# Performance work log

Measured on AMD Instinct MI355X. Metric: run time of the kernel, lower is better.

The kernel has to match this reference:

```python
import jax, jax.numpy as jnp
import numpy as np

B = 4            # scenes
N = 100000       # points per scene
BN = B * N
M = 200000       # occupied target voxels
C_IMG = 64       # img_feat_dim
C_3D = 32        # INIT_DIM (3D feature width at p1 scale)
COORD_MAX = 256  # voxel grid extent per axis


def setup_inputs() -> dict:
    key = jax.random.key(0)
    k1, k2, k3, k4, k5, k6 = jax.random.split(key, 6)
    # batched voxel coords: col0 = batch idx, cols1:4 = xyz voxel coords
    bcol = jax.random.randint(k1, (M, 1), 0, B, dtype=jnp.int32)
    xyz = jax.random.randint(k2, (M, 3), 0, COORD_MAX, dtype=jnp.int32)
    tgt_coords = jnp.concatenate([bcol, xyz], axis=1)  # (M,4)
    # each point maps onto some target voxel (torch code asserts full validity)
    pts_idx = jax.random.randint(k3, (BN,), 0, M, dtype=jnp.int32)
    pfeat = jax.random.normal(k4, (BN, C_IMG), dtype=jnp.float32)
    tgt_feats = jax.random.normal(k5, (M, C_3D), dtype=jnp.float32)
    W_fuse = jax.random.normal(k6, (C_3D + C_IMG, C_3D), dtype=jnp.float32) * 0.05
    b_fuse = jnp.zeros((C_3D,), dtype=jnp.float32)
    return {"pfeat": pfeat, "tgt_feats": tgt_feats, "W_fuse": W_fuse,
            "b_fuse": b_fuse, "tgt_coords": tgt_coords, "pts_idx": pts_idx}


def reference(pfeat, tgt_feats, W_fuse, b_fuse, tgt_coords, pts_idx):
    # point voxel coords (stride-snapped in torch; identity here since points map to voxels)
    pts_coords = tgt_coords[pts_idx]                              # (BN,4)
    # --- key packing (mirrors _pack_keys with shift-to-nonnegative) ---
    xyz_all = jnp.concatenate([pts_coords[:, 1:], tgt_coords[:, 1:]], axis=0)
    shift = jnp.maximum(-xyz_all.min(axis=0), 0)
    pts_xyz = pts_coords[:, 1:] + shift
    tgt_xyz = tgt_coords[:, 1:] + shift
    max_xyz = jnp.maximum(pts_xyz.max(axis=0), tgt_xyz.max(axis=0))
    mx, my, mz = max_xyz[0] + 1, max_xyz[1] + 1, max_xyz[2] + 1

    def pack(b, xyz):
        return ((b * mx + xyz[:, 0]) * my + xyz[:, 1]) * mz + xyz[:, 2]

    pts_key = pack(pts_coords[:, 0], pts_xyz)                     # (BN,)
    tgt_key = pack(tgt_coords[:, 0], tgt_xyz)                     # (M,)
    # --- sort target keys, binary-search point keys (torch.sort + searchsorted) ---
    order = jnp.argsort(tgt_key)
    tgt_key_sorted = tgt_key[order]
    pos = jnp.minimum(jnp.searchsorted(tgt_key_sorted, pts_key), M - 1)
    tgt_idx = order[pos]                                          # (BN,) voxel each point lands in
    # --- scatter-mean of 2D point features into voxels (_scatter_mean) ---
    sums = jax.ops.segment_sum(pfeat, tgt_idx, num_segments=M)    # (M,C_IMG)
    cnt = jax.ops.segment_sum(jnp.ones((pfeat.shape[0], 1), pfeat.dtype),
                              tgt_idx, num_segments=M)            # (M,1)
    img_feat_u = sums / jnp.maximum(cnt, 1.0)
    # --- ME.cat + 1x1 MinkowskiConvolution fuse == concat + matmul ---
    fused = jnp.concatenate([tgt_feats, img_feat_u], axis=1)      # (M, C_3D+C_IMG)
    return fused @ W_fuse + b_fuse                                # (M, C_3D)
```

## Files before the change

kernel.cpp:

```cpp
#include <hip/hip_runtime.h>

#define HBITS 19
#define HSIZE (1u << HBITS)
#define HMASK (HSIZE - 1u)
#define EMPTY_KEY 0xFFFFFFFFu
#define SLOTS 8

__device__ __forceinline__ unsigned hash_key(unsigned k) {
    return (k * 2654435761u) >> (32 - HBITS);
}

__device__ __forceinline__ unsigned pack_key(int4 c) {
    return ((unsigned)c.x << 24) | ((unsigned)c.y << 16) |
           ((unsigned)c.z << 8) | (unsigned)c.w;
}

__global__ __launch_bounds__(256)
void build_hash(const int4* __restrict__ tgt_coords, int M,
                uint2* __restrict__ htab) {
    int v = blockIdx.x * blockDim.x + threadIdx.x;
    if (v >= M) return;
    unsigned key = pack_key(tgt_coords[v]);
    unsigned h = hash_key(key);
    while (true) {
        unsigned prev = atomicCAS(&htab[h].x, EMPTY_KEY, key);
        if (prev == EMPTY_KEY || prev == key) {
            atomicMin(&htab[h].y, (unsigned)v);
            break;
        }
        h = (h + 1u) & HMASK;
    }
}

__global__ __launch_bounds__(256)
void canonize(const int4* __restrict__ tgt_coords,
              const uint2* __restrict__ htab, int M,
              int* __restrict__ canon) {
    int v = blockIdx.x * blockDim.x + threadIdx.x;
    if (v >= M) return;
    unsigned key = pack_key(tgt_coords[v]);
    unsigned h = hash_key(key);
    uint2 e = htab[h];
    while (e.x != key) { h = (h + 1u) & HMASK; e = htab[h]; }
    canon[v] = (int)e.y;
}

__global__ __launch_bounds__(256)
void fill_slots(const int* __restrict__ pts_idx,
                const int* __restrict__ canon,
                int BN,
                int* __restrict__ cnt,
                int* __restrict__ slotbuf,
                int* __restrict__ ohead,
                int* __restrict__ nxt) {
    int p = blockIdx.x * blockDim.x + threadIdx.x;
    if (p >= BN) return;
    int c = canon[pts_idx[p]];
    int idx = atomicAdd(&cnt[c], 1) + 1;
    if (idx < SLOTS) slotbuf[c * SLOTS + idx] = p;
    else             nxt[p] = atomicExch(&ohead[c], p);
}

#define VOXB 64
#define MSTR 66
#define NPASS (VOXB / 8)

struct PassRegs {
    float2 f0, f1, f2, f3, f4, f5, f6, f7;
    int n;
    int vb;
};

__device__ __forceinline__ void issue_pass(
    PassRegs& r, int pp, int grp, int g,
    const float2* __restrict__ pf2,
    const int* scnt, const int4* sslot) {
    int vb = pp * 8 + grp;
    r.vb = vb;
    int n = scnt[vb] + 1;
    r.n = n;
    int4 sa = sslot[vb * 2];
    int4 sb = sslot[vb * 2 + 1];
    int p0 = (n > 0) ? sa.x : 0;
    int p1 = (n > 1) ? sa.y : 0;
    int p2 = (n > 2) ? sa.z : 0;
    int p3 = (n > 3) ? sa.w : 0;
    int p4 = (n > 4) ? sb.x : 0;
    int p5 = (n > 5) ? sb.y : 0;
    int p6 = (n > 6) ? sb.z : 0;
    int p7 = (n > 7) ? sb.w : 0;
    r.f0 = pf2[(size_t)p0 * 32 + g];
    r.f1 = pf2[(size_t)p1 * 32 + g];
    r.f2 = pf2[(size_t)p2 * 32 + g];
    r.f3 = pf2[(size_t)p3 * 32 + g];
    r.f4 = pf2[(size_t)p4 * 32 + g];
    r.f5 = pf2[(size_t)p5 * 32 + g];
    r.f6 = pf2[(size_t)p6 * 32 + g];
    r.f7 = pf2[(size_t)p7 * 32 + g];
}

__device__ __forceinline__ void consume_pass(
    const PassRegs& r, int g, int vbase, int M,
    const float2* __restrict__ pf2,
    const int* __restrict__ ohead, const int* __restrict__ nxt,
    float (*ms)[MSTR]) {
    int v = vbase + r.vb;
    if (v >= M) return;
    int n = r.n;
    float m0 = (n > 0) ? 1.f : 0.f;
    float m1 = (n > 1) ? 1.f : 0.f;
    float m2 = (n > 2) ? 1.f : 0.f;
    float m3 = (n > 3) ? 1.f : 0.f;
    float m4 = (n > 4) ? 1.f : 0.f;
    float m5 = (n > 5) ? 1.f : 0.f;
    float m6 = (n > 6) ? 1.f : 0.f;
    float m7 = (n > 7) ? 1.f : 0.f;
    float sx = ((r.f0.x * m0 + r.f1.x * m1) + (r.f2.x * m2 + r.f3.x * m3)) +
               ((r.f4.x * m4 + r.f5.x * m5) + (r.f6.x * m6 + r.f7.x * m7));
    float sy = ((r.f0.y * m0 + r.f1.y * m1) + (r.f2.y * m2 + r.f3.y * m3)) +
               ((r.f4.y * m4 + r.f5.y * m5) + (r.f6.y * m6 + r.f7.y * m7));
    if (n > SLOTS) {
        int p = ohead[v];
        while (p >= 0) {
            float2 f = pf2[(size_t)p * 32 + g];
            sx += f.x; sy += f.y;
            p = nxt[p];
        }
    }
    float inv = 1.0f / fmaxf((float)n, 1.0f);
    *reinterpret_cast<float2*>(&ms[r.vb][2 * g]) =
        make_float2(sx * inv, sy * inv);
}

__global__ __launch_bounds__(256, 8)
void gather_fuse(const float2* __restrict__ pf2,
                 const float* __restrict__ tgtf,
                 const int* __restrict__ cnt,
                 const int4* __restrict__ slot4,
                 const int* __restrict__ ohead,
                 const int* __restrict__ nxt,
                 const float* __restrict__ W,
                 const float* __restrict__ bias,
                 int M,
                 float* __restrict__ out) {
    __shared__ __align__(16) float ms[VOXB][MSTR];
    __shared__ int scnt[VOXB];
    __shared__ __align__(16) int4 sslot[VOXB * 2];

    int t = threadIdx.x;
    int vbase = blockIdx.x * VOXB;

    if (t < VOXB) {
        int v = vbase + t;
        scnt[t] = (v < M) ? cnt[v] : -1;
    }
    if (t < VOXB * 2) {
        int j = vbase * 2 + t;
        sslot[t] = (j < M * 2) ? slot4[j] : make_int4(0, 0, 0, 0);
    }
    __syncthreads();

    int grp = t >> 5;
    int g   = t & 31;

    {
        PassRegs A, B;
        issue_pass(A, 0, grp, g, pf2, scnt, sslot);
#pragma unroll
        for (int pp = 0; pp < NPASS; pp += 2) {
            if (pp + 1 < NPASS)
                issue_pass(B, pp + 1, grp, g, pf2, scnt, sslot);
            consume_pass(A, g, vbase, M, pf2, ohead, nxt, ms);
            if (pp + 2 < NPASS)
                issue_pass(A, pp + 2, grp, g, pf2, scnt, sslot);
            if (pp + 1 < NPASS)
                consume_pass(B, g, vbase, M, pf2, ohead, nxt, ms);
        }
    }

    __syncthreads();

    int vb2 = t & (VOXB - 1);
    int ocb = __builtin_amdgcn_readfirstlane((t >> 6) << 3);
    int v2  = vbase + vb2;
    if (v2 < M) {
        float acc[8];
#pragma unroll
        for (int j = 0; j < 8; ++j) acc[j] = bias[ocb + j];

        const float4* tr = reinterpret_cast<const float4*>(tgtf + (size_t)v2 * 32);
#pragma unroll
        for (int k4 = 0; k4 < 8; ++k4) {
            float4 x = tr[k4];
            const float* w0 = W + (k4 * 4 + 0) * 32 + ocb;
            const float* w1 = W + (k4 * 4 + 1) * 32 + ocb;
            const float* w2 = W + (k4 * 4 + 2) * 32 + ocb;
            const float* w3 = W + (k4 * 4 + 3) * 32 + ocb;
#pragma unroll
            for (int j = 0; j < 8; ++j) {
                acc[j] = fmaf(x.x, w0[j], acc[j]);
                acc[j] = fmaf(x.y, w1[j], acc[j]);
                acc[j] = fmaf(x.z, w2[j], acc[j]);
                acc[j] = fmaf(x.w, w3[j], acc[j]);
            }
        }
#pragma unroll
        for (int k4 = 0; k4 < 16; ++k4) {
            float2 xa = *reinterpret_cast<const float2*>(&ms[vb2][k4 * 4]);
            float2 xb = *reinterpret_cast<const float2*>(&ms[vb2][k4 * 4 + 2]);
            const float* w0 = W + ((k4 + 8) * 4 + 0) * 32 + ocb;
            const float* w1 = W + ((k4 + 8) * 4 + 1) * 32 + ocb;
            const float* w2 = W + ((k4 + 8) * 4 + 2) * 32 + ocb;
            const float* w3 = W + ((k4 + 8) * 4 + 3) * 32 + ocb;
#pragma unroll
            for (int j = 0; j < 8; ++j) {
                acc[j] = fmaf(xa.x, w0[j], acc[j]);
                acc[j] = fmaf(xa.y, w1[j], acc[j]);
                acc[j] = fmaf(xb.x, w2[j], acc[j]);
                acc[j] = fmaf(xb.y, w3[j], acc[j]);
            }
        }

        float4* o = reinterpret_cast<float4*>(out + (size_t)v2 * 32 + ocb);
        o[0] = make_float4(acc[0], acc[1], acc[2], acc[3]);
        o[1] = make_float4(acc[4], acc[5], acc[6], acc[7]);
    }
}

extern "C" void kernel_launch(void* const* d_in, const int* in_sizes, int n_in,
                              void* d_out, int out_size, void* d_ws, size_t ws_size,
                              hipStream_t stream) {
    const float* pfeat      = (const float*)d_in[0];
    const float* tgt_feats  = (const float*)d_in[1];
    const float* W_fuse     = (const float*)d_in[2];
    const float* b_fuse     = (const float*)d_in[3];
    const int*   tgt_coords = (const int*)d_in[4];
    const int*   pts_idx    = (const int*)d_in[5];
    float* out = (float*)d_out;

    const int M  = in_sizes[4] / 4;
    const int BN = in_sizes[5];

    char* ws = (char*)d_ws;
    uint2* htab    = (uint2*)ws;
    size_t off = (size_t)HSIZE * 8;
    int*   cnt     = (int*)(ws + off);              off += (size_t)M * 4;
    int*   ohead   = (int*)(ws + off);              off += (size_t)M * 4;
    int*   canon   = (int*)(ws + off);              off += (size_t)M * 4;
    int*   slotbuf = (int*)(ws + off);              off += (size_t)M * SLOTS * 4;
    int*   nxt     = (int*)(ws + off);

    size_t ff_bytes = (size_t)HSIZE * 8 + (size_t)M * 8;
    hipMemsetAsync(htab, 0xFF, ff_bytes, stream);

    const int TB = 256;
    build_hash<<<(M + TB - 1) / TB, TB, 0, stream>>>(
        (const int4*)tgt_coords, M, htab);
    canonize<<<(M + TB - 1) / TB, TB, 0, stream>>>(
        (const int4*)tgt_coords, htab, M, canon);
    fill_slots<<<(BN + TB - 1) / TB, TB, 0, stream>>>(
        pts_idx, canon, BN, cnt, slotbuf, ohead, nxt);
    gather_fuse<<<(M + VOXB - 1) / VOXB, TB, 0, stream>>>(
        (const float2*)pfeat, tgt_feats, cnt, (const int4*)slotbuf, ohead, nxt,
        W_fuse, b_fuse, M, out);
}
```

Baseline: 270.2 us.

## Shrink per-voxel inline slots to four and process two voxels per pass

Cuts the inline slot buffer from eight to four point indices per voxel, so slot metadata is one int4 per voxel. Each warp group now handles two voxels per pass, with four feature loads per voxel, and the minimum-occupancy launch bound is dropped. The aim is less slot memory traffic and less masked-out gather work, given about two points per voxel on average. Voxels holding more than four points now take the serial linked-list overflow path more often, which adds dependent loads.

New measurement: 259.0 us. -4.1%, faster.

```diff
diff --git a/kernel.cpp b/kernel.cpp
--- a/kernel.cpp
+++ b/kernel.cpp
@@ -4,7 +4,7 @@
 #define HSIZE (1u << HBITS)
 #define HMASK (HSIZE - 1u)
 #define EMPTY_KEY 0xFFFFFFFFu
-#define SLOTS 8
+#define SLOTS 4
 
 __device__ __forceinline__ unsigned hash_key(unsigned k) {
     return (k * 2654435761u) >> (32 - HBITS);
@@ -63,62 +63,55 @@
 
 #define VOXB 64
 #define MSTR 66
-#define NPASS (VOXB / 8)
+#define NPASS (VOXB / 16)
 
 struct PassRegs {
-    float2 f0, f1, f2, f3, f4, f5, f6, f7;
-    int n;
-    int vb;
+    float2 fa0, fa1, fa2, fa3;
+    float2 fb0, fb1, fb2, fb3;
+    int na, nb;
+    int vba;
 };
 
 __device__ __forceinline__ void issue_pass(
     PassRegs& r, int pp, int grp, int g,
     const float2* __restrict__ pf2,
     const int* scnt, const int4* sslot) {
-    int vb = pp * 8 + grp;
-    r.vb = vb;
-    int n = scnt[vb] + 1;
-    r.n = n;
-    int4 sa = sslot[vb * 2];
-    int4 sb = sslot[vb * 2 + 1];
-    int p0 = (n > 0) ? sa.x : 0;
-    int p1 = (n > 1) ? sa.y : 0;
-    int p2 = (n > 2) ? sa.z : 0;
-    int p3 = (n > 3) ? sa.w : 0;
-    int p4 = (n > 4) ? sb.x : 0;
-    int p5 = (n > 5) ? sb.y : 0;
-    int p6 = (n > 6) ? sb.z : 0;
-    int p7 = (n > 7) ? sb.w : 0;
-    r.f0 = pf2[(size_t)p0 * 32 + g];
-    r.f1 = pf2[(size_t)p1 * 32 + g];
-    r.f2 = pf2[(size_t)p2 * 32 + g];
-    r.f3 = pf2[(size_t)p3 * 32 + g];
-    r.f4 = pf2[(size_t)p4 * 32 + g];
-    r.f5 = pf2[(size_t)p5 * 32 + g];
-    r.f6 = pf2[(size_t)p6 * 32 + g];
-    r.f7 = pf2[(size_t)p7 * 32 + g];
-}
-
-__device__ __forceinline__ void consume_pass(
-    const PassRegs& r, int g, int vbase, int M,
+    int vba = pp * 16 + grp * 2;
+    r.vba = vba;
+    int na = scnt[vba] + 1;
+    int nb = scnt[vba + 1] + 1;
+    r.na = na; r.nb = nb;
+    int4 sa = sslot[vba];
+    int4 sb = sslot[vba + 1];
+    int pa0 = (na > 0) ? sa.x : 0;
+    int pa1 = (na > 1) ? sa.y : 0;
+    int pa2 = (na > 2) ? sa.z : 0;
+    int pa3 = (na > 3) ? sa.w : 0;
+    int pb0 = (nb > 0) ? sb.x : 0;
+    int pb1 = (nb > 1) ? sb.y : 0;
+    int pb2 = (nb > 2) ? sb.z : 0;
+    int pb3 = (nb > 3) ? sb.w : 0;
+    r.fa0 = pf2[(size_t)pa0 * 32 + g];
+    r.fa1 = pf2[(size_t)pa1 * 32 + g];
+    r.fa2 = pf2[(size_t)pa2 * 32 + g];
+    r.fa3 = pf2[(size_t)pa3 * 32 + g];
+    r.fb0 = pf2[(size_t)pb0 * 32 + g];
+    r.fb1 = pf2[(size_t)pb1 * 32 + g];
+    r.fb2 = pf2[(size_t)pb2 * 32 + g];
+    r.fb3 = pf2[(size_t)pb3 * 32 + g];
+}
+
+__device__ __forceinline__ void sum_voxel(
+    float2 f0, float2 f1, float2 f2, float2 f3, int n, int v, int vb, int g,
     const float2* __restrict__ pf2,
     const int* __restrict__ ohead, const int* __restrict__ nxt,
     float (*ms)[MSTR]) {
-    int v = vbase + r.vb;
-    if (v >= M) return;
-    int n = r.n;
     float m0 = (n > 0) ? 1.f : 0.f;
     float m1 = (n > 1) ? 1.f : 0.f;
     float m2 = (n > 2) ? 1.f : 0.f;
     float m3 = (n > 3) ? 1.f : 0.f;
-    float m4 = (n > 4) ? 1.f : 0.f;
-    float m5 = (n > 5) ? 1.f : 0.f;
-    float m6 = (n > 6) ? 1.f : 0.f;
-    float m7 = (n > 7) ? 1.f : 0.f;
-    float sx = ((r.f0.x * m0 + r.f1.x * m1) + (r.f2.x * m2 + r.f3.x * m3)) +
-               ((r.f4.x * m4 + r.f5.x * m5) + (r.f6.x * m6 + r.f7.x * m7));
-    float sy = ((r.f0.y * m0 + r.f1.y * m1) + (r.f2.y * m2 + r.f3.y * m3)) +
-               ((r.f4.y * m4 + r.f5.y * m5) + (r.f6.y * m6 + r.f7.y * m7));
+    float sx = (f0.x * m0 + f1.x * m1) + (f2.x * m2 + f3.x * m3);
+    float sy = (f0.y * m0 + f1.y * m1) + (f2.y * m2 + f3.y * m3);
     if (n > SLOTS) {
         int p = ohead[v];
         while (p >= 0) {
@@ -128,11 +121,26 @@
         }
     }
     float inv = 1.0f / fmaxf((float)n, 1.0f);
-    *reinterpret_cast<float2*>(&ms[r.vb][2 * g]) =
+    *reinterpret_cast<float2*>(&ms[vb][2 * g]) =
         make_float2(sx * inv, sy * inv);
 }
 
-__global__ __launch_bounds__(256, 8)
+__device__ __forceinline__ void consume_pass(
+    const PassRegs& r, int g, int vbase, int M,
+    const float2* __restrict__ pf2,
+    const int* __restrict__ ohead, const int* __restrict__ nxt,
+    float (*ms)[MSTR]) {
+    int va = vbase + r.vba;
+    if (va < M)
+        sum_voxel(r.fa0, r.fa1, r.fa2, r.fa3, r.na, va, r.vba, g,
+                  pf2, ohead, nxt, ms);
+    int vb = va + 1;
+    if (vb < M)
+        sum_voxel(r.fb0, r.fb1, r.fb2, r.fb3, r.nb, vb, r.vba + 1, g,
+                  pf2, ohead, nxt, ms);
+}
+
+__global__ __launch_bounds__(256)
 void gather_fuse(const float2* __restrict__ pf2,
                  const float* __restrict__ tgtf,
                  const int* __restrict__ cnt,
@@ -145,18 +153,15 @@
                  float* __restrict__ out) {
     __shared__ __align__(16) float ms[VOXB][MSTR];
     __shared__ int scnt[VOXB];
-    __shared__ __align__(16) int4 sslot[VOXB * 2];
+    __shared__ __align__(16) int4 sslot[VOXB];
 
     int t = threadIdx.x;
     int vbase = blockIdx.x * VOXB;
 
     if (t < VOXB) {
         int v = vbase + t;
-        scnt[t] = (v < M) ? cnt[v] : -1;
-    }
-    if (t < VOXB * 2) {
-        int j = vbase * 2 + t;
-        sslot[t] = (j < M * 2) ? slot4[j] : make_int4(0, 0, 0, 0);
+        scnt[t]  = (v < M) ? cnt[v] : -1;
+        sslot[t] = (v < M) ? slot4[v] : make_int4(0, 0, 0, 0);
     }
     __syncthreads();
 
```
